# Kernel optimization log

Measured on AMD Instinct MI355X. Metric: run time of the kernel, lower is better.

Reference implementation:

```python
import jax, jax.numpy as jnp
import numpy as np

B, T, D = 2048, 60, 6
H, F, O = 64, 10, 1


def setup_inputs() -> dict:
    key = jax.random.key(0)
    ks = jax.random.split(key, 16)
    w = lambda k, shape, s=0.1: jax.random.normal(k, shape, jnp.float32) * s
    return {
        "x": jax.random.normal(ks[0], (B, T, D), jnp.float32),
        "W_i": w(ks[1], (D, H)), "U_i": w(ks[2], (H, H)), "b_i": jnp.zeros((H,), jnp.float32),
        "W_ste": w(ks[3], (D, H)), "U_ste": w(ks[4], (H, H)), "b_ste": jnp.ones((H,), jnp.float32),
        "W_fre": w(ks[5], (D, F)), "U_fre": w(ks[6], (H, F)), "b_fre": jnp.ones((F,), jnp.float32),
        "W_c": w(ks[7], (D, H)), "U_c": w(ks[8], (H, H)), "b_c": jnp.zeros((H,), jnp.float32),
        "W_o": w(ks[9], (D, H)), "U_o": w(ks[10], (H, H)), "b_o": jnp.zeros((H,), jnp.float32),
        "U_a": w(ks[11], (F, 1)), "b_a": jnp.zeros((H,), jnp.float32),
        "W_p": w(ks[12], (H, O)), "b_p": jnp.zeros((O,), jnp.float32),
    }


def _hsig(v):
    # torch.nn.Hardsigmoid: relu6(x + 3) / 6
    return jnp.clip(v / 6.0 + 0.5, 0.0, 1.0)


def reference(x, W_i, U_i, b_i, W_ste, U_ste, b_ste, W_fre, U_fre, b_fre,
              W_c, U_c, b_c, W_o, U_o, b_o, U_a, b_a, W_p, b_p):
    b, t_len, _ = x.shape
    h_dim = W_i.shape[1]
    f_dim = W_fre.shape[1]
    freq = jnp.arange(f_dim, dtype=x.dtype) / f_dim  # (F,)
    ua = U_a[:, 0]  # (F,)

    def step(carry, x_t):
        h, S_re, S_im, t = carry
        i = _hsig(x_t @ W_i + b_i + h @ U_i)              # (B,H)
        ste = _hsig(x_t @ W_ste + b_ste + h @ U_ste)      # (B,H)
        fre = _hsig(x_t @ W_fre + b_fre + h @ U_fre)      # (B,F)
        f = ste[:, :, None] * fre[:, None, :]             # (B,H,F)
        c = i * jnp.tanh(x_t @ W_c + b_c + h @ U_c)       # (B,H)
        t = t + 1.0
        omega = (2.0 * jnp.pi) * t * freq                  # (F,)
        S_re = f * S_re + c[:, :, None] * jnp.cos(omega)   # (B,H,F)
        S_im = f * S_im + c[:, :, None] * jnp.sin(omega)   # (B,H,F)
        A = S_re * S_re + S_im * S_im                      # (B,H,F)
        a = jnp.tanh(jnp.einsum('bhf,f->bh', A, ua) + b_a)
        o = _hsig(x_t @ W_o + b_o + h @ U_o)
        h = o * a
        return (h, S_re, S_im, t), None

    init = (jnp.zeros((b, h_dim), x.dtype),
            jnp.zeros((b, h_dim, f_dim), x.dtype),
            jnp.zeros((b, h_dim, f_dim), x.dtype),
            jnp.asarray(0.0, x.dtype))
    (h, _, _, _), _ = jax.lax.scan(step, init, jnp.swapaxes(x, 0, 1))
    # original returns p from the last timestep only
    return h @ W_p + b_p
```

## Files before the change

### kernel.cpp

```cpp
#include <hip/hip_runtime.h>


#define BB 2048
#define TT 60
#define DD 6
#define HH 64
#define FF 10
#define NB 4

#define XCS 964
#define HSK 72
#define ZC 68

typedef short bf16x8 __attribute__((ext_vector_type(8)));
typedef float f32x4  __attribute__((ext_vector_type(4)));

__device__ __forceinline__ unsigned short f2bf(float f) {
    union { float f; unsigned u; } v; v.f = f;
    unsigned r = v.u + 0x7fffu + ((v.u >> 16) & 1u);
    return (unsigned short)(r >> 16);
}
__device__ __forceinline__ float bf2f(unsigned short b) {
    union { unsigned u; float f; } v; v.u = ((unsigned)b) << 16; return v.f;
}
__device__ __forceinline__ float hsig_f(float v) {
    return __builtin_amdgcn_fmed3f(fmaf(v, 0.16666666666666666f, 0.5f), 0.0f, 1.0f);
}
__device__ __forceinline__ float tanh_f(float x) {
    float xc = fminf(fmaxf(x, -12.0f), 12.0f);
    float e  = __builtin_amdgcn_exp2f(xc * 2.8853900817779268f);
    return (e - 1.0f) * __builtin_amdgcn_rcpf(e + 1.0f);
}
__device__ __forceinline__ float uni(float v) {
    return __int_as_float(__builtin_amdgcn_readfirstlane(__float_as_int(v)));
}
__device__ __forceinline__ void pinv(bf16x8& v) { asm volatile("" : "+v"(v)); }

__global__ __launch_bounds__(256, 2)
void sfm_kernel(
    const float* __restrict__ x,
    const float* __restrict__ W_i,  const float* __restrict__ U_i,  const float* __restrict__ b_i,
    const float* __restrict__ W_ste,const float* __restrict__ U_ste,const float* __restrict__ b_ste,
    const float* __restrict__ W_fre,const float* __restrict__ U_fre,const float* __restrict__ b_fre,
    const float* __restrict__ W_c,  const float* __restrict__ U_c,  const float* __restrict__ b_c,
    const float* __restrict__ W_o,  const float* __restrict__ U_o,  const float* __restrict__ b_o,
    const float* __restrict__ U_a,  const float* __restrict__ b_a,
    const float* __restrict__ W_p,  const float* __restrict__ b_p,
    float* __restrict__ out)
{
    const int tid  = threadIdx.x;
    const int lane = tid & 63;
    const int wave = tid >> 6;
    const int q    = lane >> 4;
    const int n16  = lane & 15;
    const int b0   = blockIdx.x * NB;

    __shared__ __align__(16) float xc[NB * XCS];
    __shared__ __align__(16) unsigned short hsp2[16 * HSK];
    __shared__ __align__(16) float zt[4 * 8 * ZC];
    __shared__ __align__(16) float fb[NB * 12];
    __shared__ __align__(16) float ctab[10 * 10 * 2];
    __shared__ float cstabB[10 * 2];
    __shared__ float red[4][NB];

    for (int i = tid; i < NB * TT * DD; i += 256) {
        const int b = i / (TT * DD), rem = i - b * (TT * DD);
        const int s = rem / DD, d = rem - s * DD;
        xc[b * XCS + s * 16 + d] = x[(size_t)b0 * (TT * DD) + i];
    }
    if (tid < 10) {
        const float CTc[10] = { 1.0f,  0.8090169943749475f,  0.30901699437494745f,
                               -0.30901699437494745f, -0.8090169943749475f, -1.0f,
                               -0.8090169943749475f, -0.30901699437494745f,
                                0.30901699437494745f,  0.8090169943749475f };
        const float STc[10] = { 0.0f,  0.5877852522924731f,  0.9510565162951535f,
                                0.9510565162951535f,  0.5877852522924731f,  0.0f,
                               -0.5877852522924731f, -0.9510565162951535f,
                               -0.9510565162951535f, -0.5877852522924731f };
        float cc = 0.0f, ss = 0.0f;
        #pragma unroll
        for (int j = 0; j < 10; ++j) if (tid == j) { cc = CTc[j]; ss = STc[j]; }
        cstabB[tid * 2] = cc; cstabB[tid * 2 + 1] = ss;
    }
    for (int i = tid; i < 16 * HSK; i += 256) hsp2[i] = 0;
    __syncthreads();

    if (tid < NB * TT) {
        const int b = tid / TT, s = tid - b * TT;
        float xr[DD];
        #pragma unroll
        for (int d = 0; d < DD; ++d) xr[d] = xc[b * XCS + s * 16 + d];
        #pragma unroll
        for (int f = 0; f < FF; ++f) {
            float v = b_fre[f];
            #pragma unroll
            for (int d = 0; d < DD; ++d) v = fmaf(xr[d], W_fre[d * FF + f], v);
            xc[b * XCS + s * 16 + 6 + f] = v;
        }
    }
    if (tid < 100) {
        const int mm = tid / 10, ff = tid - mm * 10;
        const int idx = (ff * mm) % 10;
        ctab[tid * 2]     = cstabB[idx * 2];
        ctab[tid * 2 + 1] = cstabB[idx * 2 + 1];
    }

    const int NTILE = (wave == 0) ? 5 : 4;
    const float* Ug = (wave == 0) ? U_i : (wave == 1) ? U_ste : (wave == 2) ? U_c : U_o;
    bf16x8 Ah[5][2], Al[5][2];
    #pragma unroll
    for (int t = 0; t < 5; ++t) {
        if (t >= NTILE) continue;
        const bool isfre = (t == 4);
        #pragma unroll
        for (int c = 0; c < 2; ++c) {
            #pragma unroll
            for (int j = 0; j < 8; ++j) {
                const int kv = c * 32 + q * 8 + j;
                float v = 0.0f;
                if (!isfre)          v = Ug[kv * HH + t * 16 + n16];
                else if (n16 < FF)   v = U_fre[kv * FF + n16];
                const unsigned short hb = f2bf(v);
                Ah[t][c][j] = (short)hb;
                Al[t][c][j] = (short)f2bf(v - bf2f(hb));
            }
            pinv(Ah[t][c]); pinv(Al[t][c]);
        }
    }

    const int pb = tid & (NB - 1);
    const int pc = tid >> 2;
    const float bav = b_a[pc];
    const float wpv = W_p[pc];
    const float bpv = uni(b_p[0]);
    float uav[FF];
    #pragma unroll
    for (int f = 0; f < FF; ++f) uav[f] = uni(U_a[f]);
    float wxi[DD], wxs[DD], wxc[DD], wxo[DD];
    #pragma unroll
    for (int d = 0; d < DD; ++d) {
        wxi[d] = W_i[d * HH + pc];  wxs[d] = W_ste[d * HH + pc];
        wxc[d] = W_c[d * HH + pc];  wxo[d] = W_o[d * HH + pc];
    }
    const float bi = b_i[pc], bs = b_ste[pc], bc = b_c[pc], bo = b_o[pc];

    float Sre[FF], Sim[FF];
    #pragma unroll
    for (int f = 0; f < FF; ++f) { Sre[f] = 0.0f; Sim[f] = 0.0f; }
    float hv = 0.0f;

    const unsigned short* hrp = &hsp2[n16 * HSK];

    __syncthreads();

    int m = 1;
    for (int s = 0; s < TT; ++s) {
        const bf16x8 B0 = *(const bf16x8*)&hrp[q * 8];
        const bf16x8 B1 = *(const bf16x8*)&hrp[32 + q * 8];

        f32x4 acc[5];
        #pragma unroll
        for (int t = 0; t < 5; ++t) {
            if (t >= NTILE) continue;
            f32x4 a = {0.0f, 0.0f, 0.0f, 0.0f};
            a = __builtin_amdgcn_mfma_f32_16x16x32_bf16(Ah[t][0], B0, a, 0, 0, 0);
            a = __builtin_amdgcn_mfma_f32_16x16x32_bf16(Al[t][0], B0, a, 0, 0, 0);
            a = __builtin_amdgcn_mfma_f32_16x16x32_bf16(Ah[t][1], B1, a, 0, 0, 0);
            a = __builtin_amdgcn_mfma_f32_16x16x32_bf16(Al[t][1], B1, a, 0, 0, 0);
            acc[t] = a;
        }

        if (n16 < 8) {
            #pragma unroll
            for (int t = 0; t < 4; ++t)
                *(f32x4*)&zt[(wave * 8 + n16) * ZC + t * 16 + q * 4] = acc[t];
        }
        if (wave == 0) {
            f32x4 af;
            #pragma unroll
            for (int r = 0; r < 4; ++r)
                af[r] = acc[4][r] + __shfl_xor(acc[4][r], 4, 64);
            if (n16 < 4) {
                #pragma unroll
                for (int r = 0; r < 4; ++r) {
                    const int f = q * 4 + r;
                    if (f < FF) fb[n16 * 12 + f] = af[r] + xc[n16 * XCS + s * 16 + 6 + f];
                }
            }
        }
        __syncthreads();

        const float4 xv4 = *(const float4*)&xc[pb * XCS + s * 16];
        const float2 xv2 = *(const float2*)&xc[pb * XCS + s * 16 + 4];
        const float xa[DD] = {xv4.x, xv4.y, xv4.z, xv4.w, xv2.x, xv2.y};

        float vi = bi, vs = bs, vc = bc, vo = bo;
        #pragma unroll
        for (int d = 0; d < DD; ++d) {
            vi = fmaf(xa[d], wxi[d], vi);
            vs = fmaf(xa[d], wxs[d], vs);
            vc = fmaf(xa[d], wxc[d], vc);
            vo = fmaf(xa[d], wxo[d], vo);
        }
        const float zi = zt[(0 * 8 + pb) * ZC + pc] + zt[(0 * 8 + pb + 4) * ZC + pc] + vi;
        const float zs = zt[(1 * 8 + pb) * ZC + pc] + zt[(1 * 8 + pb + 4) * ZC + pc] + vs;
        const float zc = zt[(2 * 8 + pb) * ZC + pc] + zt[(2 * 8 + pb + 4) * ZC + pc] + vc;
        const float zo = zt[(3 * 8 + pb) * ZC + pc] + zt[(3 * 8 + pb + 4) * ZC + pc] + vo;

        float fr[FF];
        #pragma unroll
        for (int f = 0; f < FF; ++f) fr[f] = hsig_f(fb[pb * 12 + f]);

        const float iv  = hsig_f(zi);
        const float stv = hsig_f(zs);
        const float ov  = hsig_f(zo);
        const float cv  = iv * tanh_f(zc);

        const float* tp = &ctab[m * 20];
        float aacc0 = bav, aacc1 = 0.0f;
        #pragma unroll
        for (int f = 0; f < FF; ++f) {
            const float2 tv = *(const float2*)&tp[f * 2];
            const float fc = stv * fr[f];
            Sre[f] = fmaf(fc, Sre[f], cv * tv.x);
            Sim[f] = fmaf(fc, Sim[f], cv * tv.y);
            const float A = fmaf(Sim[f], Sim[f], Sre[f] * Sre[f]);
            if (f & 1) aacc1 = fmaf(A, uav[f], aacc1);
            else       aacc0 = fmaf(A, uav[f], aacc0);
        }
        hv = ov * tanh_f(aacc0 + aacc1);

        {
            const unsigned short hb = f2bf(hv);
            hsp2[pb * HSK + pc]       = hb;
            hsp2[(4 + pb) * HSK + pc] = f2bf(hv - bf2f(hb));
        }
        if (++m == 10) m = 0;
        __syncthreads();
    }

    float val = hv * wpv;
    val += __shfl_xor(val, 4, 64);
    val += __shfl_xor(val, 8, 64);
    val += __shfl_xor(val, 16, 64);
    val += __shfl_xor(val, 32, 64);
    if (lane < NB) red[wave][lane] = val;
    __syncthreads();
    if (tid < NB)
        out[b0 + tid] = red[0][tid] + red[1][tid] + red[2][tid] + red[3][tid] + bpv;
}

extern "C" void kernel_launch(void* const* d_in, const int* in_sizes, int n_in,
                              void* d_out, int out_size, void* d_ws, size_t ws_size,
                              hipStream_t stream) {
    (void)in_sizes; (void)n_in; (void)d_ws; (void)ws_size; (void)out_size;
    const float* x     = (const float*)d_in[0];
    const float* W_i   = (const float*)d_in[1];
    const float* U_i   = (const float*)d_in[2];
    const float* b_i   = (const float*)d_in[3];
    const float* W_ste = (const float*)d_in[4];
    const float* U_ste = (const float*)d_in[5];
    const float* b_ste = (const float*)d_in[6];
    const float* W_fre = (const float*)d_in[7];
    const float* U_fre = (const float*)d_in[8];
    const float* b_fre = (const float*)d_in[9];
    const float* W_c   = (const float*)d_in[10];
    const float* U_c   = (const float*)d_in[11];
    const float* b_c   = (const float*)d_in[12];
    const float* W_o   = (const float*)d_in[13];
    const float* U_o   = (const float*)d_in[14];
    const float* b_o   = (const float*)d_in[15];
    const float* U_a   = (const float*)d_in[16];
    const float* b_a   = (const float*)d_in[17];
    const float* W_p   = (const float*)d_in[18];
    const float* b_p   = (const float*)d_in[19];

    sfm_kernel<<<BB / NB, 256, 0, stream>>>(
        x, W_i, U_i, b_i, W_ste, U_ste, b_ste, W_fre, U_fre, b_fre,
        W_c, U_c, b_c, W_o, U_o, b_o, U_a, b_a, W_p, b_p, (float*)d_out);
}
```

Before: 169.7 us.

## Split waves into MFMA producers and pointwise consumers with ping-pong batch groups

Result: slower. 183.5 us (+8.1%).

```diff
diff --git a/kernel.cpp b/kernel.cpp
--- a/kernel.cpp
+++ b/kernel.cpp
@@ -6,11 +6,11 @@
 #define DD 6
 #define HH 64
 #define FF 10
-#define NB 4
+#define NB 8
 
 #define XCS 964
 #define HSK 72
-#define ZC 68
+#define ZS 68
 
 typedef short bf16x8 __attribute__((ext_vector_type(8)));
 typedef float f32x4  __attribute__((ext_vector_type(4)));
@@ -36,7 +36,7 @@
 }
 __device__ __forceinline__ void pinv(bf16x8& v) { asm volatile("" : "+v"(v)); }
 
-__global__ __launch_bounds__(256, 2)
+__global__ __launch_bounds__(512, 1)
 void sfm_kernel(
     const float* __restrict__ x,
     const float* __restrict__ W_i,  const float* __restrict__ U_i,  const float* __restrict__ b_i,
@@ -56,14 +56,15 @@
     const int b0   = blockIdx.x * NB;
 
     __shared__ __align__(16) float xc[NB * XCS];
-    __shared__ __align__(16) unsigned short hsp2[16 * HSK];
-    __shared__ __align__(16) float zt[4 * 8 * ZC];
-    __shared__ __align__(16) float fb[NB * 12];
+    __shared__ __align__(16) unsigned short hsp[24 * HSK];
+    __shared__ __align__(16) float zA[4 * 4 * ZS];
+    __shared__ __align__(16) float zB[4 * 4 * ZS];
+    __shared__ __align__(16) float fbA[4 * 12];
+    __shared__ __align__(16) float fbB[4 * 12];
     __shared__ __align__(16) float ctab[10 * 10 * 2];
     __shared__ float cstabB[10 * 2];
-    __shared__ float red[4][NB];
-
-    for (int i = tid; i < NB * TT * DD; i += 256) {
+
+    for (int i = tid; i < NB * TT * DD; i += 512) {
         const int b = i / (TT * DD), rem = i - b * (TT * DD);
         const int s = rem / DD, d = rem - s * DD;
         xc[b * XCS + s * 16 + d] = x[(size_t)b0 * (TT * DD) + i];
@@ -82,7 +83,7 @@
         for (int j = 0; j < 10; ++j) if (tid == j) { cc = CTc[j]; ss = STc[j]; }
         cstabB[tid * 2] = cc; cstabB[tid * 2 + 1] = ss;
     }
-    for (int i = tid; i < 16 * HSK; i += 256) hsp2[i] = 0;
+    for (int i = tid; i < 24 * HSK; i += 512) hsp[i] = 0;
     __syncthreads();
 
     if (tid < NB * TT) {
@@ -105,149 +106,182 @@
         ctab[tid * 2 + 1] = cstabB[idx * 2 + 1];
     }
 
-    const int NTILE = (wave == 0) ? 5 : 4;
-    const float* Ug = (wave == 0) ? U_i : (wave == 1) ? U_ste : (wave == 2) ? U_c : U_o;
-    bf16x8 Ah[5][2], Al[5][2];
-    #pragma unroll
-    for (int t = 0; t < 5; ++t) {
-        if (t >= NTILE) continue;
-        const bool isfre = (t == 4);
+    if (wave < 4) {
+        const int w = wave;
+        const float* Ug = (w == 0) ? U_i : (w == 1) ? U_ste : (w == 2) ? U_c : U_o;
+
+        bf16x8 Ah[4][2], Al[4][2], Fh[2], Fl[2];
+        #pragma unroll
+        for (int t = 0; t < 4; ++t) {
+            #pragma unroll
+            for (int c = 0; c < 2; ++c) {
+                #pragma unroll
+                for (int j = 0; j < 8; ++j) {
+                    const int kv = c * 32 + q * 8 + j;
+                    const float v = Ug[kv * HH + t * 16 + n16];
+                    const unsigned short hb = f2bf(v);
+                    Ah[t][c][j] = (short)hb;
+                    Al[t][c][j] = (short)f2bf(v - bf2f(hb));
+                }
+                pinv(Ah[t][c]); pinv(Al[t][c]);
+            }
+        }
         #pragma unroll
         for (int c = 0; c < 2; ++c) {
             #pragma unroll
             for (int j = 0; j < 8; ++j) {
                 const int kv = c * 32 + q * 8 + j;
-                float v = 0.0f;
-                if (!isfre)          v = Ug[kv * HH + t * 16 + n16];
-                else if (n16 < FF)   v = U_fre[kv * FF + n16];
+                const float v = (n16 < FF) ? U_fre[kv * FF + n16] : 0.0f;
                 const unsigned short hb = f2bf(v);
-                Ah[t][c][j] = (short)hb;
-                Al[t][c][j] = (short)f2bf(v - bf2f(hb));
-            }
-            pinv(Ah[t][c]); pinv(Al[t][c]);
-        }
-    }
-
-    const int pb = tid & (NB - 1);
-    const int pc = tid >> 2;
-    const float bav = b_a[pc];
-    const float wpv = W_p[pc];
-    const float bpv = uni(b_p[0]);
-    float uav[FF];
-    #pragma unroll
-    for (int f = 0; f < FF; ++f) uav[f] = uni(U_a[f]);
-    float wxi[DD], wxs[DD], wxc[DD], wxo[DD];
-    #pragma unroll
-    for (int d = 0; d < DD; ++d) {
-        wxi[d] = W_i[d * HH + pc];  wxs[d] = W_ste[d * HH + pc];
-        wxc[d] = W_c[d * HH + pc];  wxo[d] = W_o[d * HH + pc];
-    }
-    const float bi = b_i[pc], bs = b_ste[pc], bc = b_c[pc], bo = b_o[pc];
-
-    float Sre[FF], Sim[FF];
-    #pragma unroll
-    for (int f = 0; f < FF; ++f) { Sre[f] = 0.0f; Sim[f] = 0.0f; }
-    float hv = 0.0f;
-
-    const unsigned short* hrp = &hsp2[n16 * HSK];
-
-    __syncthreads();
-
-    int m = 1;
-    for (int s = 0; s < TT; ++s) {
-        const bf16x8 B0 = *(const bf16x8*)&hrp[q * 8];
-        const bf16x8 B1 = *(const bf16x8*)&hrp[32 + q * 8];
-
-        f32x4 acc[5];
-        #pragma unroll
-        for (int t = 0; t < 5; ++t) {
-            if (t >= NTILE) continue;
-            f32x4 a = {0.0f, 0.0f, 0.0f, 0.0f};
-            a = __builtin_amdgcn_mfma_f32_16x16x32_bf16(Ah[t][0], B0, a, 0, 0, 0);
-            a = __builtin_amdgcn_mfma_f32_16x16x32_bf16(Al[t][0], B0, a, 0, 0, 0);
-            a = __builtin_amdgcn_mfma_f32_16x16x32_bf16(Ah[t][1], B1, a, 0, 0, 0);
-            a = __builtin_amdgcn_mfma_f32_16x16x32_bf16(Al[t][1], B1, a, 0, 0, 0);
-            acc[t] = a;
-        }
-
-        if (n16 < 8) {
-            #pragma unroll
-            for (int t = 0; t < 4; ++t)
-                *(f32x4*)&zt[(wave * 8 + n16) * ZC + t * 16 + q * 4] = acc[t];
-        }
-        if (wave == 0) {
-            f32x4 af;
-            #pragma unroll
-            for (int r = 0; r < 4; ++r)
-                af[r] = acc[4][r] + __shfl_xor(acc[4][r], 4, 64);
-            if (n16 < 4) {
+                Fh[c][j] = (short)hb;
+                Fl[c][j] = (short)f2bf(v - bf2f(hb));
+            }
+            pinv(Fh[c]); pinv(Fl[c]);
+        }
+
+        const unsigned short* hrpA = &hsp[((n16 < 8) ? n16       : (16 + n16 - 8)) * HSK];
+        const unsigned short* hrpB = &hsp[((n16 < 8) ? (8 + n16) : (16 + n16 - 8)) * HSK];
+
+        auto do_M = [&](const unsigned short* hrp, float* zg, float* fb,
+                        const int gbase, const int s) {
+            const bf16x8 B0 = *(const bf16x8*)&hrp[q * 8];
+            const bf16x8 B1 = *(const bf16x8*)&hrp[32 + q * 8];
+            #pragma unroll
+            for (int t = 0; t < 4; ++t) {
+                f32x4 a = {0.0f, 0.0f, 0.0f, 0.0f};
+                a = __builtin_amdgcn_mfma_f32_16x16x32_bf16(Ah[t][0], B0, a, 0, 0, 0);
+                a = __builtin_amdgcn_mfma_f32_16x16x32_bf16(Al[t][0], B0, a, 0, 0, 0);
+                a = __builtin_amdgcn_mfma_f32_16x16x32_bf16(Ah[t][1], B1, a, 0, 0, 0);
+                a = __builtin_amdgcn_mfma_f32_16x16x32_bf16(Al[t][1], B1, a, 0, 0, 0);
+                f32x4 z;
                 #pragma unroll
-                for (int r = 0; r < 4; ++r) {
-                    const int f = q * 4 + r;
-                    if (f < FF) fb[n16 * 12 + f] = af[r] + xc[n16 * XCS + s * 16 + 6 + f];
+                for (int r = 0; r < 4; ++r)
+                    z[r] = a[r] + __shfl_xor(a[r], 4, 64);
+                if (n16 < 4)
+                    *(f32x4*)&zg[(w * 4 + n16) * ZS + t * 16 + q * 4] = z;
+            }
+            if (w == 0) {
+                f32x4 a = {0.0f, 0.0f, 0.0f, 0.0f};
+                a = __builtin_amdgcn_mfma_f32_16x16x32_bf16(Fh[0], B0, a, 0, 0, 0);
+                a = __builtin_amdgcn_mfma_f32_16x16x32_bf16(Fl[0], B0, a, 0, 0, 0);
+                a = __builtin_amdgcn_mfma_f32_16x16x32_bf16(Fh[1], B1, a, 0, 0, 0);
+                a = __builtin_amdgcn_mfma_f32_16x16x32_bf16(Fl[1], B1, a, 0, 0, 0);
+                f32x4 z;
+                #pragma unroll
+                for (int r = 0; r < 4; ++r)
+                    z[r] = a[r] + __shfl_xor(a[r], 4, 64);
+                if (n16 < 4) {
+                    #pragma unroll
+                    for (int r = 0; r < 4; ++r) {
+                        const int f = q * 4 + r;
+                        if (f < FF)
+                            fb[n16 * 12 + f] = z[r] + xc[(gbase + n16) * XCS + s * 16 + 6 + f];
+                    }
                 }
             }
-        }
+        };
+
+        do_M(hrpA, zA, fbA, 0, 0);
         __syncthreads();
 
-        const float4 xv4 = *(const float4*)&xc[pb * XCS + s * 16];
-        const float2 xv2 = *(const float2*)&xc[pb * XCS + s * 16 + 4];
-        const float xa[DD] = {xv4.x, xv4.y, xv4.z, xv4.w, xv2.x, xv2.y};
-
-        float vi = bi, vs = bs, vc = bc, vo = bo;
+        for (int s = 0; s < TT; ++s) {
+            do_M(hrpB, zB, fbB, 4, s);
+            __syncthreads();
+            if (s + 1 < TT)
+                do_M(hrpA, zA, fbA, 0, s + 1);
+            __syncthreads();
+        }
+    } else {
+        const int p  = wave - 4;
+        const int hc = lane;
+        const float bav = b_a[hc];
+        const float wpv = W_p[hc];
+        const float bpv = uni(b_p[0]);
+        float uav[FF];
+        #pragma unroll
+        for (int f = 0; f < FF; ++f) uav[f] = uni(U_a[f]);
+        float wxi[DD], wxs[DD], wxc[DD], wxo[DD];
         #pragma unroll
         for (int d = 0; d < DD; ++d) {
-            vi = fmaf(xa[d], wxi[d], vi);
-            vs = fmaf(xa[d], wxs[d], vs);
-            vc = fmaf(xa[d], wxc[d], vc);
-            vo = fmaf(xa[d], wxo[d], vo);
-        }
-        const float zi = zt[(0 * 8 + pb) * ZC + pc] + zt[(0 * 8 + pb + 4) * ZC + pc] + vi;
-        const float zs = zt[(1 * 8 + pb) * ZC + pc] + zt[(1 * 8 + pb + 4) * ZC + pc] + vs;
-        const float zc = zt[(2 * 8 + pb) * ZC + pc] + zt[(2 * 8 + pb + 4) * ZC + pc] + vc;
-        const float zo = zt[(3 * 8 + pb) * ZC + pc] + zt[(3 * 8 + pb + 4) * ZC + pc] + vo;
-
-        float fr[FF];
-        #pragma unroll
-        for (int f = 0; f < FF; ++f) fr[f] = hsig_f(fb[pb * 12 + f]);
-
-        const float iv  = hsig_f(zi);
-        const float stv = hsig_f(zs);
-        const float ov  = hsig_f(zo);
-        const float cv  = iv * tanh_f(zc);
-
-        const float* tp = &ctab[m * 20];
-        float aacc0 = bav, aacc1 = 0.0f;
-        #pragma unroll
-        for (int f = 0; f < FF; ++f) {
-            const float2 tv = *(const float2*)&tp[f * 2];
-            const float fc = stv * fr[f];
-            Sre[f] = fmaf(fc, Sre[f], cv * tv.x);
-            Sim[f] = fmaf(fc, Sim[f], cv * tv.y);
-            const float A = fmaf(Sim[f], Sim[f], Sre[f] * Sre[f]);
-            if (f & 1) aacc1 = fmaf(A, uav[f], aacc1);
-            else       aacc0 = fmaf(A, uav[f], aacc0);
-        }
-        hv = ov * tanh_f(aacc0 + aacc1);
-
-        {
+            wxi[d] = W_i[d * HH + hc];  wxs[d] = W_ste[d * HH + hc];
+            wxc[d] = W_c[d * HH + hc];  wxo[d] = W_o[d * HH + hc];
+        }
+        const float bi = b_i[hc], bs = b_ste[hc], bc = b_c[hc], bo = b_o[hc];
+
+        float SreA[FF], SimA[FF], SreB[FF], SimB[FF];
+        #pragma unroll
+        for (int f = 0; f < FF; ++f) { SreA[f]=0.f; SimA[f]=0.f; SreB[f]=0.f; SimB[f]=0.f; }
+        float hvA = 0.0f, hvB = 0.0f;
+
+        auto do_P = [&](const float* zg, const float* fb, float* Sre, float* Sim,
+                        const int bglob, const int grow, const int s,
+                        const float* tp) -> float {
+            const float* xr = &xc[bglob * XCS + s * 16];
+            float vi = bi, vs = bs, vc = bc, vo = bo;
+            #pragma unroll
+            for (int d = 0; d < DD; ++d) {
+                const float xd = xr[d];
+                vi = fmaf(xd, wxi[d], vi);
+                vs = fmaf(xd, wxs[d], vs);
+                vc = fmaf(xd, wxc[d], vc);
+                vo = fmaf(xd, wxo[d], vo);
+            }
+            const float zi = zg[(0 * 4 + p) * ZS + hc] + vi;
+            const float zs = zg[(1 * 4 + p) * ZS + hc] + vs;
+            const float zc = zg[(2 * 4 + p) * ZS + hc] + vc;
+            const float zo = zg[(3 * 4 + p) * ZS + hc] + vo;
+
+            float fr[FF];
+            #pragma unroll
+            for (int f = 0; f < FF; ++f) fr[f] = hsig_f(fb[p * 12 + f]);
+
+            const float iv  = hsig_f(zi);
+            const float stv = hsig_f(zs);
+            const float ov  = hsig_f(zo);
+            const float cv  = iv * tanh_f(zc);
+
+            float a0 = bav, a1 = 0.0f;
+            #pragma unroll
+            for (int f = 0; f < FF; ++f) {
+                const float2 tv = *(const float2*)&tp[f * 2];
+                const float fc = stv * fr[f];
+                Sre[f] = fmaf(fc, Sre[f], cv * tv.x);
+                Sim[f] = fmaf(fc, Sim[f], cv * tv.y);
+                const float A = fmaf(Sim[f], Sim[f], Sre[f] * Sre[f]);
+                if (f & 1) a1 = fmaf(A, uav[f], a1);
+                else       a0 = fmaf(A, uav[f], a0);
+            }
+            const float hv = ov * tanh_f(a0 + a1);
             const unsigned short hb = f2bf(hv);
-            hsp2[pb * HSK + pc]       = hb;
-            hsp2[(4 + pb) * HSK + pc] = f2bf(hv - bf2f(hb));
-        }
-        if (++m == 10) m = 0;
+            hsp[(grow + p) * HSK + hc]     = hb;
+            hsp[(grow + 4 + p) * HSK + hc] = f2bf(hv - bf2f(hb));
+            return hv;
+        };
+
         __syncthreads();
-    }
-
-    float val = hv * wpv;
-    val += __shfl_xor(val, 4, 64);
-    val += __shfl_xor(val, 8, 64);
-    val += __shfl_xor(val, 16, 64);
-    val += __shfl_xor(val, 32, 64);
-    if (lane < NB) red[wave][lane] = val;
-    __syncthreads();
-    if (tid < NB)
-        out[b0 + tid] = red[0][tid] + red[1][tid] + red[2][tid] + red[3][tid] + bpv;
+
+        int m = 1;
+        for (int s = 0; s < TT; ++s) {
+            const float* tp = &ctab[m * 20];
+            hvA = do_P(zA, fbA, SreA, SimA, p, 0, s, tp);
+            __syncthreads();
+            hvB = do_P(zB, fbB, SreB, SimB, 4 + p, 8, s, tp);
+            __syncthreads();
+            if (++m == 10) m = 0;
+        }
+
+        float vA = hvA * wpv, vB = hvB * wpv;
+        #pragma unroll
+        for (int off = 32; off > 0; off >>= 1) {
+            vA += __shfl_xor(vA, off, 64);
+            vB += __shfl_xor(vB, off, 64);
+        }
+        if (lane == 0) {
+            out[b0 + p]     = vA + bpv;
+            out[b0 + 4 + p] = vB + bpv;
+        }
+        return;
+    }
 }
 
 extern "C" void kernel_launch(void* const* d_in, const int* in_sizes, int n_in,
@@ -275,7 +309,7 @@
     const float* W_p   = (const float*)d_in[18];
     const float* b_p   = (const float*)d_in[19];
 
-    sfm_kernel<<<BB / NB, 256, 0, stream>>>(
+    sfm_kernel<<<BB / NB, 512, 0, stream>>>(
         x, W_i, U_i, b_i, W_ste, U_ste, b_ste, W_fre, U_fre, b_fre,
         W_c, U_c, b_c, W_o, U_o, b_o, U_a, b_a, W_p, b_p, (float*)d_out);
 }
```
